# Kernel tuning notes

Hardware: AMD Instinct MI355X
Metric: run time of the kernel (lower is better)

The kernel has to match this reference:

```python
import jax, jax.numpy as jnp
import numpy as np

VOX = 64      # vox_size
KS = 21       # smooth_ks (odd -> 'SAME' == pad ks//2)
SIGMA = 3.0   # smooth_sigma


def smoothing_kernel():
    # normalized 1D gaussian used separably along the 3 voxel axes
    x = jnp.arange(KS, dtype=jnp.float32) - (KS - 1) / 2.0
    g = jnp.exp(-(x * x) / (2.0 * SIGMA * SIGMA))
    return g / g.sum()


def pc_voxels(pc, size):
    """Trilinear scatter of points in [-0.5,0.5]^3 into a [B,size,size,size] grid."""
    B, N, _ = pc.shape
    g = (pc + 0.5) * (size - 1)            # grid coords
    fl = jnp.floor(g)
    idx = fl.astype(jnp.int32)             # [B,N,3] lower corner
    frac = g - fl                          # trilinear fractions
    # 8 corner offsets in {0,1}^3
    offs = jnp.array([[(i >> 2) & 1, (i >> 1) & 1, i & 1] for i in range(8)], dtype=jnp.int32)
    pos = idx[:, :, None, :] + offs[None, None]                       # [B,N,8,3]
    w = jnp.prod(jnp.where(offs[None, None].astype(bool),
                           frac[:, :, None, :], 1.0 - frac[:, :, None, :]), axis=-1)  # [B,N,8]
    inb = jnp.all((pos >= 0) & (pos < size), axis=-1)
    w = jnp.where(inb, w, 0.0)
    posc = jnp.clip(pos, 0, size - 1)
    # voxel layout vox[b, z, y, x]; pc columns are (x, y, z)
    flat = posc[..., 2] * (size * size) + posc[..., 1] * size + posc[..., 0]
    vox = jnp.zeros((B, size * size * size), pc.dtype)
    vox = vox.at[jnp.arange(B)[:, None, None], flat].add(w)
    return jnp.clip(vox.reshape(B, size, size, size), 0.0, 1.0)


def voxels_smooth(v, g1d, scale):
    """Separable 3D Gaussian smoothing + per-batch scale, clamped to [0,1]."""
    x = v[:, None]  # NCDHW, C=1
    ks = g1d.shape[0]
    for kshape in ((1, 1, ks, 1, 1), (1, 1, 1, ks, 1), (1, 1, 1, 1, ks)):
        x = jax.lax.conv_general_dilated(
            x, g1d.reshape(kshape), (1, 1, 1), 'SAME',
            dimension_numbers=('NCDHW', 'OIDHW', 'NCDHW'))
    x = x[:, 0] * scale[:, None, None, None]
    return jnp.clip(x, 0.0, 1.0)


def drc_prob(v):
    """DRC ray-termination probabilities along depth (axis 1)."""
    trans = jnp.cumprod(1.0 - v, axis=1)                                   # [B,D,H,W]
    tshift = jnp.concatenate([jnp.ones_like(trans[:, :1]), trans[:, :-1]], axis=1)
    stop = v * tshift                                                      # stop at voxel d
    esc = trans[:, -1:]                                                    # ray escapes
    return jnp.concatenate([stop, esc], axis=1)                            # [B,D+1,H,W]


def reference(pc, rotation, scale):
    pc_t = jnp.einsum('bni,bji->bnj', pc, rotation)   # camera transform: pc @ R^T
    vox = pc_voxels(pc_t, VOX)
    sm = voxels_smooth(vox, smoothing_kernel(), scale)
    prob = drc_prob(sm)
    proj = prob[:, :-1].sum(1)[:, ::-1, :]            # sum over depth, flip rows
    return proj


def setup_inputs() -> dict:
    key = jax.random.key(0)
    k1, k2, k3 = jax.random.split(key, 3)
    B, N = 32, 65536
    pc = jax.random.uniform(k1, (B, N, 3), jnp.float32) - 0.5   # points in [-0.5, 0.5]
    q, _ = jnp.linalg.qr(jax.random.normal(k2, (B, 3, 3), jnp.float32))  # random rotations
    scale = 0.5 + jax.random.uniform(k3, (B,), jnp.float32)
    return {"pc": pc, "rotation": q, "scale": scale}
```

## Files before the change

kernel.cpp:

```cpp
#include <hip/hip_runtime.h>

#define NB    32
#define NP    65536
#define SZ    64
#define SZ3   (SZ * SZ * SZ)
#define KS    21
#define HALF  10
#define NBIN2 130
#define CAP2  1280
#define FXS   960.0f

typedef _Float16 half8_t __attribute__((ext_vector_type(8)));
typedef _Float16 half4_t __attribute__((ext_vector_type(4)));
typedef float    f32x4_t __attribute__((ext_vector_type(4)));

__device__ __forceinline__ int swz(int row, int col) {
    return (row << 6) + ((((col >> 3) ^ (row & 7))) << 3) + (col & 7);
}

__device__ __forceinline__ void weights_reg(float* w) {
    float sum = 0.0f;
#pragma unroll
    for (int k = 0; k < KS; ++k) {
        float d = (float)k - (float)HALF;
        w[k] = expf(-d * d / 18.0f);
        sum += w[k];
    }
#pragma unroll
    for (int k = 0; k < KS; ++k) w[k] /= sum;
}

__device__ __forceinline__ void fma4(float4& a, float t, const float4& v) {
    a.x = fmaf(t, v.x, a.x); a.y = fmaf(t, v.y, a.y);
    a.z = fmaf(t, v.z, a.z); a.w = fmaf(t, v.w, a.w);
}

__device__ __forceinline__ unsigned pack_fx(float g) {
    float c = fminf(fmaxf(g, -2.0f), 65.0f);
    return (unsigned)__float2uint_rn((c + 2.0f) * FXS);
}

__global__ void fill_kernel(const float* __restrict__ pc,
                            const float* __restrict__ rot,
                            int* __restrict__ cur,
                            uint2* __restrict__ binned,
                            _Float16* __restrict__ Gg) {
    __shared__ int h[4][NBIN2];
    __shared__ int woff[4][NBIN2];
    __shared__ int lbase[NBIN2];
    int base = blockIdx.x * 1024;
    int b = base >> 16;
    int wv = threadIdx.x >> 6;
    for (int i = threadIdx.x; i < 4 * NBIN2; i += 256) h[i / NBIN2][i % NBIN2] = 0;
    __syncthreads();
    const float* R = rot + b * 9;
    const float4* p4 = (const float4*)(pc + (size_t)base * 3);
    float4 f0 = p4[threadIdx.x * 3 + 0];
    float4 f1 = p4[threadIdx.x * 3 + 1];
    float4 f2 = p4[threadIdx.x * 3 + 2];
    float px[4] = {f0.x, f0.w, f1.z, f2.y};
    float py[4] = {f0.y, f1.x, f1.w, f2.z};
    float pz[4] = {f0.z, f1.y, f2.x, f2.w};
    uint2 pk[4];
    int bin0[4], bin1[4], lp0[4], lp1[4];
#pragma unroll
    for (int j = 0; j < 4; ++j) {
        float g0 = (R[0] * px[j] + R[1] * py[j] + R[2] * pz[j] + 0.5f) * 63.0f;
        float g1 = (R[3] * px[j] + R[4] * py[j] + R[5] * pz[j] + 0.5f) * 63.0f;
        float g2 = (R[6] * px[j] + R[7] * py[j] + R[8] * pz[j] + 0.5f) * 63.0f;
        int i2 = (int)floorf(g2);
        int i1 = (int)floorf(g1);
        bool zv = (i2 >= -1 && i2 <= 63);
        int h0 = ((unsigned)i1       < 64u) ? (i1 >> 5)       : -1;
        int h1 = ((unsigned)(i1 + 1) < 64u) ? ((i1 + 1) >> 5) : -1;
        if (h1 == h0) h1 = -1;
        bin0[j] = (zv && h0 >= 0) ? ((i2 + 1) * 2 + h0) : -1;
        bin1[j] = (zv && h1 >= 0) ? ((i2 + 1) * 2 + h1) : -1;
        pk[j] = make_uint2(pack_fx(g0) | (pack_fx(g1) << 16), pack_fx(g2));
        if (bin0[j] >= 0) lp0[j] = atomicAdd(&h[wv][bin0[j]], 1);
        if (bin1[j] >= 0) lp1[j] = atomicAdd(&h[wv][bin1[j]], 1);
    }
    __syncthreads();
    if (threadIdx.x < NBIN2) {
        int t = threadIdx.x;
        int s0 = h[0][t], s1 = h[1][t], s2 = h[2][t], s3 = h[3][t];
        int tot = s0 + s1 + s2 + s3;
        lbase[t] = tot ? atomicAdd(&cur[b * NBIN2 + t], tot) : 0;
        woff[0][t] = 0; woff[1][t] = s0; woff[2][t] = s0 + s1; woff[3][t] = s0 + s1 + s2;
    }
    __syncthreads();
#pragma unroll
    for (int j = 0; j < 4; ++j) {
        if (bin0[j] >= 0) {
            int pos = lbase[bin0[j]] + woff[wv][bin0[j]] + lp0[j];
            if (pos < CAP2)
                binned[(size_t)(b * NBIN2 + bin0[j]) * CAP2 + pos] = pk[j];
        }
        if (bin1[j] >= 0) {
            int pos = lbase[bin1[j]] + woff[wv][bin1[j]] + lp1[j];
            if (pos < CAP2)
                binned[(size_t)(b * NBIN2 + bin1[j]) * CAP2 + pos] = pk[j];
        }
    }
    if (blockIdx.x == 0) {
        float w[KS];
        weights_reg(w);
        for (int i = threadIdx.x; i < 4096; i += 256) {
            int d = (i >> 6) - (i & 63) + HALF;
            Gg[i] = ((unsigned)d < (unsigned)KS) ? (_Float16)w[d] : (_Float16)0.0f;
        }
    }
}

__global__ void __launch_bounds__(128) splat_blur(const uint2* __restrict__ binned,
                                                  const int* __restrict__ cur,
                                                  const _Float16* __restrict__ Gg,
                                                  _Float16* __restrict__ vox) {
    __shared__ __align__(16) char smem[25088];
    int tid = threadIdx.x;
    int w = tid >> 6, lane = tid & 63;
    int idx = blockIdx.x;
    int b = idx >> 6;
    int k = (idx + (b << 3)) & 63;
    int z = (k & 1) ? (31 - (k >> 1)) : (32 + (k >> 1));
    int q = lane >> 4, c = lane & 15;

    _Float16* Ay = (_Float16*)(smem + w * 4224);
    _Float16* Bx = (_Float16*)(smem + 8448 + w * 8320);
    _Float16* P  = (_Float16*)smem;
    _Float16* T  = (_Float16*)(smem + 8448);

    {
        int4 z4 = {0, 0, 0, 0};
        int4* a4 = (int4*)Ay;
        for (int i = lane; i < 4224 / 16; i += 64) a4[i] = z4;
        int4* b4 = (int4*)Bx;
        for (int i = lane; i < 8320 / 16; i += 64) b4[i] = z4;
    }

    half8_t gf[4][2];
#pragma unroll
    for (int ni = 0; ni < 4; ++ni)
#pragma unroll
        for (int hh = 0; hh < 2; ++hh)
            gf[ni][hh] = *(const half8_t*)&Gg[(ni * 16 + c) * 64 + hh * 32 + q * 8];

    int c0 = min(cur[b * NBIN2 + 2 * z + w],       CAP2);
    int c1 = min(cur[b * NBIN2 + 2 * (z + 1) + w], CAP2);
    const uint2* s0 = binned + (size_t)(b * NBIN2 + 2 * z + w) * CAP2;
    const uint2* s1 = binned + (size_t)(b * NBIN2 + 2 * (z + 1) + w) * CAP2;
    int n = c0 + c1;

    f32x4_t acc[2][4];
#pragma unroll
    for (int ml = 0; ml < 2; ++ml)
#pragma unroll
        for (int ni = 0; ni < 4; ++ni) acc[ml][ni] = (f32x4_t){0.f, 0.f, 0.f, 0.f};

    int iters = (n + 63) >> 6;
    uint2 nxtA = make_uint2(0u, 0u), nxtB = make_uint2(0u, 0u);
    {
        int i0g = lane;
        if (i0g < n) nxtA = (i0g < c0) ? s0[i0g] : s1[i0g - c0];
        int i1g = 64 + lane;
        if (i1g < n) nxtB = (i1g < c0) ? s0[i1g] : s1[i1g - c0];
    }
    for (int it = 0; it < iters; ++it) {
        uint2 pk = nxtA;
        nxtA = nxtB;
        nxtB = make_uint2(0u, 0u);
        int ni2 = (it + 2) * 64 + lane;
        if (ni2 < n) nxtB = (ni2 < c0) ? s0[ni2] : s1[ni2 - c0];

        float gx = (float)(pk.x & 0xffffu) * (1.0f / FXS) - 2.0f;
        float gy = (float)(pk.x >> 16)     * (1.0f / FXS) - 2.0f;
        float gz = (float)(pk.y & 0xffffu) * (1.0f / FXS) - 2.0f;
        float f0 = floorf(gx), f1 = floorf(gy);
        int   i0 = (int)f0,    i1 = (int)f1;
        float r0 = gx - f0,    r1f = gy - f1;
        float az = fmaxf(0.0f, 1.0f - fabsf(gz - (float)z));
        int rlo = i1 - (w << 5), rhi = i1 + 1 - (w << 5);
        int alo = ((unsigned)rlo < 32u) ? rlo : 32;
        int ahi = ((unsigned)rhi < 32u) ? rhi : 32;
        int xlo = ((unsigned)i0       < 64u) ? i0       : 64;
        int xhi = ((unsigned)(i0 + 1) < 64u) ? (i0 + 1) : 64;
        Ay[swz(alo, lane)] = (_Float16)(az * (1.0f - r1f));
        Ay[swz(ahi, lane)] = (_Float16)(az * r1f);
        Bx[swz(xlo, lane)] = (_Float16)(1.0f - r0);
        Bx[swz(xhi, lane)] = (_Float16)r0;
#pragma unroll
        for (int hh = 0; hh < 2; ++hh) {
            half8_t af[2], bf[4];
#pragma unroll
            for (int ml = 0; ml < 2; ++ml)
                af[ml] = *(const half8_t*)&Ay[swz(ml * 16 + c, hh * 32 + q * 8)];
#pragma unroll
            for (int ni = 0; ni < 4; ++ni)
                bf[ni] = *(const half8_t*)&Bx[swz(ni * 16 + c, hh * 32 + q * 8)];
#pragma unroll
            for (int ml = 0; ml < 2; ++ml)
#pragma unroll
                for (int ni = 0; ni < 4; ++ni)
                    acc[ml][ni] = __builtin_amdgcn_mfma_f32_16x16x32_f16(
                        af[ml], bf[ni], acc[ml][ni], 0, 0, 0);
        }
        Ay[swz(alo, lane)] = (_Float16)0.0f;
        Ay[swz(ahi, lane)] = (_Float16)0.0f;
        Bx[swz(xlo, lane)] = (_Float16)0.0f;
        Bx[swz(xhi, lane)] = (_Float16)0.0f;
    }

    __syncthreads();

#pragma unroll
    for (int ml = 0; ml < 2; ++ml)
#pragma unroll
        for (int ni = 0; ni < 4; ++ni)
#pragma unroll
            for (int r = 0; r < 4; ++r)
                P[swz((w << 5) + ml * 16 + q * 4 + r, ni * 16 + c)] =
                    (_Float16)fminf(fmaxf(acc[ml][ni][r], 0.0f), 1.0f);
    __syncthreads();

    f32x4_t a2[2][4];
#pragma unroll
    for (int ml = 0; ml < 2; ++ml)
#pragma unroll
        for (int ni = 0; ni < 4; ++ni) a2[ml][ni] = (f32x4_t){0.f, 0.f, 0.f, 0.f};
#pragma unroll
    for (int hh = 0; hh < 2; ++hh) {
        half8_t af[2];
#pragma unroll
        for (int ml = 0; ml < 2; ++ml)
            af[ml] = *(const half8_t*)&P[swz(((w << 1) + ml) * 16 + c, hh * 32 + q * 8)];
#pragma unroll
        for (int ml = 0; ml < 2; ++ml)
#pragma unroll
            for (int ni = 0; ni < 4; ++ni)
                a2[ml][ni] = __builtin_amdgcn_mfma_f32_16x16x32_f16(
                    af[ml], gf[ni][hh], a2[ml][ni], 0, 0, 0);
    }
#pragma unroll
    for (int ml = 0; ml < 2; ++ml)
#pragma unroll
        for (int ni = 0; ni < 4; ++ni) {
            half4_t pkd;
#pragma unroll
            for (int r = 0; r < 4; ++r) pkd[r] = (_Float16)a2[ml][ni][r];
            *(half4_t*)&T[swz(ni * 16 + c, ((w << 1) + ml) * 16 + q * 4)] = pkd;
        }
    __syncthreads();

    f32x4_t a3[2][4];
#pragma unroll
    for (int ml = 0; ml < 2; ++ml)
#pragma unroll
        for (int ni = 0; ni < 4; ++ni) a3[ml][ni] = (f32x4_t){0.f, 0.f, 0.f, 0.f};
#pragma unroll
    for (int hh = 0; hh < 2; ++hh) {
        half8_t bf[4];
#pragma unroll
        for (int ni = 0; ni < 4; ++ni)
            bf[ni] = *(const half8_t*)&T[swz(ni * 16 + c, hh * 32 + q * 8)];
#pragma unroll
        for (int ml = 0; ml < 2; ++ml)
#pragma unroll
            for (int ni = 0; ni < 4; ++ni)
                a3[ml][ni] = __builtin_amdgcn_mfma_f32_16x16x32_f16(
                    gf[(w << 1) + ml][hh], bf[ni], a3[ml][ni], 0, 0, 0);
    }

    _Float16* dst = vox + ((size_t)b << 18) + ((size_t)z << 12);
#pragma unroll
    for (int ml = 0; ml < 2; ++ml)
#pragma unroll
        for (int ni = 0; ni < 4; ++ni)
#pragma unroll
            for (int r = 0; r < 4; ++r)
                dst[(((w << 5) + ml * 16 + q * 4 + r) << 6) + ni * 16 + c] =
                    (_Float16)a3[ml][ni][r];
}

__global__ void convz_drc_kernel(const _Float16* __restrict__ in,
                                 const float* __restrict__ scale,
                                 float* __restrict__ out) {
    __shared__ float sraw[640 + SZ * SZ + 640];
    __shared__ float c[SZ * SZ];
    __shared__ float segS[4][64], segT[4][64];
    float* s = sraw + 640;
    int b = blockIdx.x >> 6, y = blockIdx.x & 63;

    for (int i = threadIdx.x; i < 640; i += 256) {
        sraw[i] = 0.0f;
        sraw[640 + SZ * SZ + i] = 0.0f;
    }
    const _Float16* base = in + ((size_t)b << 18) + (y << 6);
#pragma unroll
    for (int g = 0; g < 4; ++g) {
        int cell = g * 256 + threadIdx.x;
        int z = cell >> 4, xc = (cell & 15) << 2;
        half4_t v = *(const half4_t*)&base[((size_t)z << 12) + xc];
        float4 f = make_float4((float)v[0], (float)v[1], (float)v[2], (float)v[3]);
        *(float4*)&s[(z << 6) + xc] = f;
    }
    __syncthreads();

    float w[KS];
    weights_reg(w);

    {
        int z0 = (threadIdx.x >> 4) << 2;
        int xc = (threadIdx.x & 15) << 2;
        float4 a0 = {0,0,0,0}, a1 = {0,0,0,0}, a2 = {0,0,0,0}, a3 = {0,0,0,0};
#pragma unroll
        for (int d = 0; d < 24; ++d) {
            int zz = z0 - HALF + d;
            float4 v = *(const float4*)&s[(zz << 6) + xc];
            if (d <= 20)           fma4(a0, w[d],     v);
            if (d >= 1 && d <= 21) fma4(a1, w[d - 1], v);
            if (d >= 2 && d <= 22) fma4(a2, w[d - 2], v);
            if (d >= 3)            fma4(a3, w[d - 3], v);
        }
        *(float4*)&c[((z0 + 0) << 6) + xc] = a0;
        *(float4*)&c[((z0 + 1) << 6) + xc] = a1;
        *(float4*)&c[((z0 + 2) << 6) + xc] = a2;
        *(float4*)&c[((z0 + 3) << 6) + xc] = a3;
    }
    __syncthreads();

    {
        int x = threadIdx.x & 63, seg = threadIdx.x >> 6;
        float sc = scale[b];
        float trans = 1.0f, sum = 0.0f;
#pragma unroll
        for (int zz = 0; zz < 16; ++zz) {
            int z = seg * 16 + zz;
            float v = fminf(fmaxf(c[(z << 6) + x] * sc, 0.0f), 1.0f);
            sum += v * trans;
            trans *= 1.0f - v;
        }
        segS[seg][x] = sum;
        segT[seg][x] = trans;
    }
    __syncthreads();
    if (threadIdx.x < 64) {
        int x = threadIdx.x;
        float t = 1.0f, S = 0.0f;
#pragma unroll
        for (int sgi = 0; sgi < 4; ++sgi) { S += segS[sgi][x] * t; t *= segT[sgi][x]; }
        out[(b << 12) + ((63 - y) << 6) + x] = S;
    }
}

extern "C" void kernel_launch(void* const* d_in, const int* in_sizes, int n_in,
                              void* d_out, int out_size, void* d_ws, size_t ws_size,
                              hipStream_t stream) {
    const float* pc    = (const float*)d_in[0];
    const float* rot   = (const float*)d_in[1];
    const float* scale = (const float*)d_in[2];
    float* out = (float*)d_out;

    _Float16* vox    = (_Float16*)d_ws;
    uint2*    binned = (uint2*)((char*)d_ws + (size_t)NB * SZ3 * sizeof(_Float16));
    _Float16* Gg     = (_Float16*)((char*)binned + (size_t)NB * NBIN2 * CAP2 * sizeof(uint2));
    int*      cur    = (int*)((char*)Gg + 64 * 64 * sizeof(_Float16));

    hipMemsetAsync(cur, 0, NB * NBIN2 * sizeof(int), stream);

    fill_kernel     <<<NB * NP / 1024, 256, 0, stream>>>(pc, rot, cur, binned, Gg);
    splat_blur      <<<NB * SZ, 128, 0, stream>>>(binned, cur, Gg, vox);
    convz_drc_kernel<<<NB * SZ, 256, 0, stream>>>(vox, scale, out);
}
```

Before: 121.7 us.

## Bin points into y/x quadrants and use four waves per slice in splat_blur

```diff
diff --git a/kernel.cpp b/kernel.cpp
--- a/kernel.cpp
+++ b/kernel.cpp
@@ -6,8 +6,8 @@
 #define SZ3   (SZ * SZ * SZ)
 #define KS    21
 #define HALF  10
-#define NBIN2 130
-#define CAP2  1280
+#define NBIN4 260
+#define CAP4  1024
 #define FXS   960.0f
 
 typedef _Float16 half8_t __attribute__((ext_vector_type(8)));
@@ -45,13 +45,13 @@
                             int* __restrict__ cur,
                             uint2* __restrict__ binned,
                             _Float16* __restrict__ Gg) {
-    __shared__ int h[4][NBIN2];
-    __shared__ int woff[4][NBIN2];
-    __shared__ int lbase[NBIN2];
+    __shared__ int h[4][NBIN4];
+    __shared__ int woff[4][NBIN4];
+    __shared__ int lbase[NBIN4];
     int base = blockIdx.x * 1024;
     int b = base >> 16;
     int wv = threadIdx.x >> 6;
-    for (int i = threadIdx.x; i < 4 * NBIN2; i += 256) h[i / NBIN2][i % NBIN2] = 0;
+    for (int i = threadIdx.x; i < 4 * NBIN4; i += 256) h[i / NBIN4][i % NBIN4] = 0;
     __syncthreads();
     const float* R = rot + b * 9;
     const float4* p4 = (const float4*)(pc + (size_t)base * 3);
@@ -62,7 +62,7 @@
     float py[4] = {f0.y, f1.x, f1.w, f2.z};
     float pz[4] = {f0.z, f1.y, f2.x, f2.w};
     uint2 pk[4];
-    int bin0[4], bin1[4], lp0[4], lp1[4];
+    int bn[4][4], lp[4][4];
 #pragma unroll
     for (int j = 0; j < 4; ++j) {
         float g0 = (R[0] * px[j] + R[1] * py[j] + R[2] * pz[j] + 0.5f) * 63.0f;
@@ -70,36 +70,41 @@
         float g2 = (R[6] * px[j] + R[7] * py[j] + R[8] * pz[j] + 0.5f) * 63.0f;
         int i2 = (int)floorf(g2);
         int i1 = (int)floorf(g1);
+        int i0 = (int)floorf(g0);
         bool zv = (i2 >= -1 && i2 <= 63);
         int h0 = ((unsigned)i1       < 64u) ? (i1 >> 5)       : -1;
         int h1 = ((unsigned)(i1 + 1) < 64u) ? ((i1 + 1) >> 5) : -1;
         if (h1 == h0) h1 = -1;
-        bin0[j] = (zv && h0 >= 0) ? ((i2 + 1) * 2 + h0) : -1;
-        bin1[j] = (zv && h1 >= 0) ? ((i2 + 1) * 2 + h1) : -1;
+        int v0 = ((unsigned)i0       < 64u) ? (i0 >> 5)       : -1;
+        int v1 = ((unsigned)(i0 + 1) < 64u) ? ((i0 + 1) >> 5) : -1;
+        if (v1 == v0) v1 = -1;
+        int zb = (i2 + 1) * 2;
+        bn[j][0] = (zv && h0 >= 0 && v0 >= 0) ? ((zb + h0) * 2 + v0) : -1;
+        bn[j][1] = (zv && h0 >= 0 && v1 >= 0) ? ((zb + h0) * 2 + v1) : -1;
+        bn[j][2] = (zv && h1 >= 0 && v0 >= 0) ? ((zb + h1) * 2 + v0) : -1;
+        bn[j][3] = (zv && h1 >= 0 && v1 >= 0) ? ((zb + h1) * 2 + v1) : -1;
         pk[j] = make_uint2(pack_fx(g0) | (pack_fx(g1) << 16), pack_fx(g2));
-        if (bin0[j] >= 0) lp0[j] = atomicAdd(&h[wv][bin0[j]], 1);
-        if (bin1[j] >= 0) lp1[j] = atomicAdd(&h[wv][bin1[j]], 1);
-    }
-    __syncthreads();
-    if (threadIdx.x < NBIN2) {
-        int t = threadIdx.x;
+#pragma unroll
+        for (int t = 0; t < 4; ++t)
+            if (bn[j][t] >= 0) lp[j][t] = atomicAdd(&h[wv][bn[j][t]], 1);
+    }
+    __syncthreads();
+    for (int t = threadIdx.x; t < NBIN4; t += 256) {
         int s0 = h[0][t], s1 = h[1][t], s2 = h[2][t], s3 = h[3][t];
         int tot = s0 + s1 + s2 + s3;
-        lbase[t] = tot ? atomicAdd(&cur[b * NBIN2 + t], tot) : 0;
+        lbase[t] = tot ? atomicAdd(&cur[b * NBIN4 + t], tot) : 0;
         woff[0][t] = 0; woff[1][t] = s0; woff[2][t] = s0 + s1; woff[3][t] = s0 + s1 + s2;
     }
     __syncthreads();
 #pragma unroll
     for (int j = 0; j < 4; ++j) {
-        if (bin0[j] >= 0) {
-            int pos = lbase[bin0[j]] + woff[wv][bin0[j]] + lp0[j];
-            if (pos < CAP2)
-                binned[(size_t)(b * NBIN2 + bin0[j]) * CAP2 + pos] = pk[j];
-        }
-        if (bin1[j] >= 0) {
-            int pos = lbase[bin1[j]] + woff[wv][bin1[j]] + lp1[j];
-            if (pos < CAP2)
-                binned[(size_t)(b * NBIN2 + bin1[j]) * CAP2 + pos] = pk[j];
+#pragma unroll
+        for (int t = 0; t < 4; ++t) {
+            if (bn[j][t] >= 0) {
+                int pos = lbase[bn[j][t]] + woff[wv][bn[j][t]] + lp[j][t];
+                if (pos < CAP4)
+                    binned[(size_t)(b * NBIN4 + bn[j][t]) * CAP4 + pos] = pk[j];
+            }
         }
     }
     if (blockIdx.x == 0) {
@@ -112,13 +117,14 @@
     }
 }
 
-__global__ void __launch_bounds__(128) splat_blur(const uint2* __restrict__ binned,
-                                                  const int* __restrict__ cur,
-                                                  const _Float16* __restrict__ Gg,
-                                                  _Float16* __restrict__ vox) {
-    __shared__ __align__(16) char smem[25088];
+__global__ void __launch_bounds__(256, 4) splat_blur(const uint2* __restrict__ binned,
+                                                     const int* __restrict__ cur,
+                                                     const _Float16* __restrict__ Gg,
+                                                     _Float16* __restrict__ vox) {
+    __shared__ __align__(16) char smem[33792];
     int tid = threadIdx.x;
     int w = tid >> 6, lane = tid & 63;
+    int yh = w >> 1, xh = w & 1;
     int idx = blockIdx.x;
     int b = idx >> 6;
     int k = (idx + (b << 3)) & 63;
@@ -126,36 +132,31 @@
     int q = lane >> 4, c = lane & 15;
 
     _Float16* Ay = (_Float16*)(smem + w * 4224);
-    _Float16* Bx = (_Float16*)(smem + 8448 + w * 8320);
+    _Float16* Bx = (_Float16*)(smem + 16896 + w * 4224);
     _Float16* P  = (_Float16*)smem;
-    _Float16* T  = (_Float16*)(smem + 8448);
+    _Float16* T  = (_Float16*)(smem + 16896);
 
     {
         int4 z4 = {0, 0, 0, 0};
         int4* a4 = (int4*)Ay;
         for (int i = lane; i < 4224 / 16; i += 64) a4[i] = z4;
         int4* b4 = (int4*)Bx;
-        for (int i = lane; i < 8320 / 16; i += 64) b4[i] = z4;
-    }
-
-    half8_t gf[4][2];
-#pragma unroll
-    for (int ni = 0; ni < 4; ++ni)
-#pragma unroll
-        for (int hh = 0; hh < 2; ++hh)
-            gf[ni][hh] = *(const half8_t*)&Gg[(ni * 16 + c) * 64 + hh * 32 + q * 8];
-
-    int c0 = min(cur[b * NBIN2 + 2 * z + w],       CAP2);
-    int c1 = min(cur[b * NBIN2 + 2 * (z + 1) + w], CAP2);
-    const uint2* s0 = binned + (size_t)(b * NBIN2 + 2 * z + w) * CAP2;
-    const uint2* s1 = binned + (size_t)(b * NBIN2 + 2 * (z + 1) + w) * CAP2;
+        for (int i = lane; i < 4224 / 16; i += 64) b4[i] = z4;
+    }
+
+    int bin0 = (2 * z + yh) * 2 + xh;
+    int bin1 = (2 * (z + 1) + yh) * 2 + xh;
+    int c0 = min(cur[b * NBIN4 + bin0], CAP4);
+    int c1 = min(cur[b * NBIN4 + bin1], CAP4);
+    const uint2* s0 = binned + (size_t)(b * NBIN4 + bin0) * CAP4;
+    const uint2* s1 = binned + (size_t)(b * NBIN4 + bin1) * CAP4;
     int n = c0 + c1;
 
-    f32x4_t acc[2][4];
+    f32x4_t acc[2][2];
 #pragma unroll
     for (int ml = 0; ml < 2; ++ml)
 #pragma unroll
-        for (int ni = 0; ni < 4; ++ni) acc[ml][ni] = (f32x4_t){0.f, 0.f, 0.f, 0.f};
+        for (int ni = 0; ni < 2; ++ni) acc[ml][ni] = (f32x4_t){0.f, 0.f, 0.f, 0.f};
 
     int iters = (n + 63) >> 6;
     uint2 nxtA = make_uint2(0u, 0u), nxtB = make_uint2(0u, 0u);
@@ -179,28 +180,29 @@
         int   i0 = (int)f0,    i1 = (int)f1;
         float r0 = gx - f0,    r1f = gy - f1;
         float az = fmaxf(0.0f, 1.0f - fabsf(gz - (float)z));
-        int rlo = i1 - (w << 5), rhi = i1 + 1 - (w << 5);
+        int rlo = i1 - (yh << 5), rhi = rlo + 1;
         int alo = ((unsigned)rlo < 32u) ? rlo : 32;
         int ahi = ((unsigned)rhi < 32u) ? rhi : 32;
-        int xlo = ((unsigned)i0       < 64u) ? i0       : 64;
-        int xhi = ((unsigned)(i0 + 1) < 64u) ? (i0 + 1) : 64;
+        int xg  = i0 - (xh << 5);
+        int xlo = ((unsigned)xg       < 32u) ? xg       : 32;
+        int xhi = ((unsigned)(xg + 1) < 32u) ? (xg + 1) : 32;
         Ay[swz(alo, lane)] = (_Float16)(az * (1.0f - r1f));
         Ay[swz(ahi, lane)] = (_Float16)(az * r1f);
         Bx[swz(xlo, lane)] = (_Float16)(1.0f - r0);
         Bx[swz(xhi, lane)] = (_Float16)r0;
 #pragma unroll
         for (int hh = 0; hh < 2; ++hh) {
-            half8_t af[2], bf[4];
+            half8_t af[2], bf[2];
 #pragma unroll
             for (int ml = 0; ml < 2; ++ml)
                 af[ml] = *(const half8_t*)&Ay[swz(ml * 16 + c, hh * 32 + q * 8)];
 #pragma unroll
-            for (int ni = 0; ni < 4; ++ni)
+            for (int ni = 0; ni < 2; ++ni)
                 bf[ni] = *(const half8_t*)&Bx[swz(ni * 16 + c, hh * 32 + q * 8)];
 #pragma unroll
             for (int ml = 0; ml < 2; ++ml)
 #pragma unroll
-                for (int ni = 0; ni < 4; ++ni)
+                for (int ni = 0; ni < 2; ++ni)
                     acc[ml][ni] = __builtin_amdgcn_mfma_f32_16x16x32_f16(
                         af[ml], bf[ni], acc[ml][ni], 0, 0, 0);
         }
@@ -212,73 +214,64 @@
 
     __syncthreads();
 
+    half8_t gf[4][2];
+#pragma unroll
+    for (int ni = 0; ni < 4; ++ni)
+#pragma unroll
+        for (int hh = 0; hh < 2; ++hh)
+            gf[ni][hh] = *(const half8_t*)&Gg[(ni * 16 + c) * 64 + hh * 32 + q * 8];
+
 #pragma unroll
     for (int ml = 0; ml < 2; ++ml)
 #pragma unroll
+        for (int ni = 0; ni < 2; ++ni)
+#pragma unroll
+            for (int r = 0; r < 4; ++r)
+                P[swz((yh << 5) + ml * 16 + q * 4 + r, (xh << 5) + ni * 16 + c)] =
+                    (_Float16)fminf(fmaxf(acc[ml][ni][r], 0.0f), 1.0f);
+    __syncthreads();
+
+    f32x4_t a2[4];
+#pragma unroll
+    for (int ni = 0; ni < 4; ++ni) a2[ni] = (f32x4_t){0.f, 0.f, 0.f, 0.f};
+#pragma unroll
+    for (int hh = 0; hh < 2; ++hh) {
+        half8_t af1 = *(const half8_t*)&P[swz(w * 16 + c, hh * 32 + q * 8)];
+#pragma unroll
         for (int ni = 0; ni < 4; ++ni)
-#pragma unroll
-            for (int r = 0; r < 4; ++r)
-                P[swz((w << 5) + ml * 16 + q * 4 + r, ni * 16 + c)] =
-                    (_Float16)fminf(fmaxf(acc[ml][ni][r], 0.0f), 1.0f);
-    __syncthreads();
-
-    f32x4_t a2[2][4];
-#pragma unroll
-    for (int ml = 0; ml < 2; ++ml)
-#pragma unroll
-        for (int ni = 0; ni < 4; ++ni) a2[ml][ni] = (f32x4_t){0.f, 0.f, 0.f, 0.f};
+            a2[ni] = __builtin_amdgcn_mfma_f32_16x16x32_f16(
+                af1, gf[ni][hh], a2[ni], 0, 0, 0);
+    }
+#pragma unroll
+    for (int ni = 0; ni < 4; ++ni) {
+        half4_t pkd;
+#pragma unroll
+        for (int r = 0; r < 4; ++r) pkd[r] = (_Float16)a2[ni][r];
+        *(half4_t*)&T[swz(ni * 16 + c, w * 16 + q * 4)] = pkd;
+    }
+    __syncthreads();
+
+    f32x4_t a3[4];
+#pragma unroll
+    for (int ni = 0; ni < 4; ++ni) a3[ni] = (f32x4_t){0.f, 0.f, 0.f, 0.f};
 #pragma unroll
     for (int hh = 0; hh < 2; ++hh) {
-        half8_t af[2];
-#pragma unroll
-        for (int ml = 0; ml < 2; ++ml)
-            af[ml] = *(const half8_t*)&P[swz(((w << 1) + ml) * 16 + c, hh * 32 + q * 8)];
-#pragma unroll
-        for (int ml = 0; ml < 2; ++ml)
-#pragma unroll
-            for (int ni = 0; ni < 4; ++ni)
-                a2[ml][ni] = __builtin_amdgcn_mfma_f32_16x16x32_f16(
-                    af[ml], gf[ni][hh], a2[ml][ni], 0, 0, 0);
-    }
-#pragma unroll
-    for (int ml = 0; ml < 2; ++ml)
-#pragma unroll
-        for (int ni = 0; ni < 4; ++ni) {
-            half4_t pkd;
-#pragma unroll
-            for (int r = 0; r < 4; ++r) pkd[r] = (_Float16)a2[ml][ni][r];
-            *(half4_t*)&T[swz(ni * 16 + c, ((w << 1) + ml) * 16 + q * 4)] = pkd;
-        }
-    __syncthreads();
-
-    f32x4_t a3[2][4];
-#pragma unroll
-    for (int ml = 0; ml < 2; ++ml)
-#pragma unroll
-        for (int ni = 0; ni < 4; ++ni) a3[ml][ni] = (f32x4_t){0.f, 0.f, 0.f, 0.f};
-#pragma unroll
-    for (int hh = 0; hh < 2; ++hh) {
-        half8_t bf[4];
+        half8_t bf1[4];
 #pragma unroll
         for (int ni = 0; ni < 4; ++ni)
-            bf[ni] = *(const half8_t*)&T[swz(ni * 16 + c, hh * 32 + q * 8)];
-#pragma unroll
-        for (int ml = 0; ml < 2; ++ml)
-#pragma unroll
-            for (int ni = 0; ni < 4; ++ni)
-                a3[ml][ni] = __builtin_amdgcn_mfma_f32_16x16x32_f16(
-                    gf[(w << 1) + ml][hh], bf[ni], a3[ml][ni], 0, 0, 0);
+            bf1[ni] = *(const half8_t*)&T[swz(ni * 16 + c, hh * 32 + q * 8)];
+#pragma unroll
+        for (int ni = 0; ni < 4; ++ni)
+            a3[ni] = __builtin_amdgcn_mfma_f32_16x16x32_f16(
+                gf[w][hh], bf1[ni], a3[ni], 0, 0, 0);
     }
 
     _Float16* dst = vox + ((size_t)b << 18) + ((size_t)z << 12);
 #pragma unroll
-    for (int ml = 0; ml < 2; ++ml)
-#pragma unroll
-        for (int ni = 0; ni < 4; ++ni)
-#pragma unroll
-            for (int r = 0; r < 4; ++r)
-                dst[(((w << 5) + ml * 16 + q * 4 + r) << 6) + ni * 16 + c] =
-                    (_Float16)a3[ml][ni][r];
+    for (int ni = 0; ni < 4; ++ni)
+#pragma unroll
+        for (int r = 0; r < 4; ++r)
+            dst[((w * 16 + q * 4 + r) << 6) + ni * 16 + c] = (_Float16)a3[ni][r];
 }
 
 __global__ void convz_drc_kernel(const _Float16* __restrict__ in,
@@ -362,12 +355,12 @@
 
     _Float16* vox    = (_Float16*)d_ws;
     uint2*    binned = (uint2*)((char*)d_ws + (size_t)NB * SZ3 * sizeof(_Float16));
-    _Float16* Gg     = (_Float16*)((char*)binned + (size_t)NB * NBIN2 * CAP2 * sizeof(uint2));
+    _Float16* Gg     = (_Float16*)((char*)binned + (size_t)NB * NBIN4 * CAP4 * sizeof(uint2));
     int*      cur    = (int*)((char*)Gg + 64 * 64 * sizeof(_Float16));
 
-    hipMemsetAsync(cur, 0, NB * NBIN2 * sizeof(int), stream);
+    hipMemsetAsync(cur, 0, NB * NBIN4 * sizeof(int), stream);
 
     fill_kernel     <<<NB * NP / 1024, 256, 0, stream>>>(pc, rot, cur, binned, Gg);
-    splat_blur      <<<NB * SZ, 128, 0, stream>>>(binned, cur, Gg, vox);
+    splat_blur      <<<NB * SZ, 256, 0, stream>>>(binned, cur, Gg, vox);
     convz_drc_kernel<<<NB * SZ, 256, 0, stream>>>(vox, scale, out);
 }
```

After: 137.0 us. +12.6%, slower.

## Precompute splat indices and fp16 weights in fill kernel, shrinking splat inner loop

Applied to the files above, without the earlier changes.

```diff
diff --git a/kernel.cpp b/kernel.cpp
--- a/kernel.cpp
+++ b/kernel.cpp
@@ -8,14 +8,17 @@
 #define HALF  10
 #define NBIN2 130
 #define CAP2  1280
-#define FXS   960.0f
 
 typedef _Float16 half8_t __attribute__((ext_vector_type(8)));
 typedef _Float16 half4_t __attribute__((ext_vector_type(4)));
+typedef _Float16 half2_t __attribute__((ext_vector_type(2)));
 typedef float    f32x4_t __attribute__((ext_vector_type(4)));
 
 __device__ __forceinline__ int swz(int row, int col) {
     return (row << 6) + ((((col >> 3) ^ (row & 7))) << 3) + (col & 7);
+}
+__device__ __forceinline__ int swzl(int row, int lane) {
+    return (((row << 6) | ((row & 7) << 3)) ^ lane);
 }
 
 __device__ __forceinline__ void weights_reg(float* w) {
@@ -35,15 +38,15 @@
     a.z = fmaf(t, v.z, a.z); a.w = fmaf(t, v.w, a.w);
 }
 
-__device__ __forceinline__ unsigned pack_fx(float g) {
-    float c = fminf(fmaxf(g, -2.0f), 65.0f);
-    return (unsigned)__float2uint_rn((c + 2.0f) * FXS);
+__device__ __forceinline__ unsigned h16(float x) {
+    _Float16 h = (_Float16)x;
+    return (unsigned)__builtin_bit_cast(unsigned short, h);
 }
 
 __global__ void fill_kernel(const float* __restrict__ pc,
                             const float* __restrict__ rot,
                             int* __restrict__ cur,
-                            uint2* __restrict__ binned,
+                            uint4* __restrict__ binned,
                             _Float16* __restrict__ Gg) {
     __shared__ int h[4][NBIN2];
     __shared__ int woff[4][NBIN2];
@@ -61,22 +64,38 @@
     float px[4] = {f0.x, f0.w, f1.z, f2.y};
     float py[4] = {f0.y, f1.x, f1.w, f2.z};
     float pz[4] = {f0.z, f1.y, f2.x, f2.w};
-    uint2 pk[4];
+    uint4 pk[4][2];
     int bin0[4], bin1[4], lp0[4], lp1[4];
 #pragma unroll
     for (int j = 0; j < 4; ++j) {
         float g0 = (R[0] * px[j] + R[1] * py[j] + R[2] * pz[j] + 0.5f) * 63.0f;
         float g1 = (R[3] * px[j] + R[4] * py[j] + R[5] * pz[j] + 0.5f) * 63.0f;
         float g2 = (R[6] * px[j] + R[7] * py[j] + R[8] * pz[j] + 0.5f) * 63.0f;
-        int i2 = (int)floorf(g2);
-        int i1 = (int)floorf(g1);
+        float fl0 = floorf(g0), fl1 = floorf(g1), fl2 = floorf(g2);
+        int i0 = (int)fl0, i1 = (int)fl1, i2 = (int)fl2;
+        float r0 = g0 - fl0, r1 = g1 - fl1, fz = g2 - fl2;
         bool zv = (i2 >= -1 && i2 <= 63);
         int h0 = ((unsigned)i1       < 64u) ? (i1 >> 5)       : -1;
         int h1 = ((unsigned)(i1 + 1) < 64u) ? ((i1 + 1) >> 5) : -1;
         if (h1 == h0) h1 = -1;
         bin0[j] = (zv && h0 >= 0) ? ((i2 + 1) * 2 + h0) : -1;
         bin1[j] = (zv && h1 >= 0) ? ((i2 + 1) * 2 + h1) : -1;
-        pk[j] = make_uint2(pack_fx(g0) | (pack_fx(g1) << 16), pack_fx(g2));
+
+        int xlo = ((unsigned)i0       < 64u) ? i0       : 64;
+        int xhi = ((unsigned)(i0 + 1) < 64u) ? (i0 + 1) : 64;
+        unsigned xw = ((unsigned)xlo << 16) | ((unsigned)xhi << 24);
+        unsigned ey = h16(fz)        | (h16(1.0f - fz) << 16);
+        unsigned ez = h16(1.0f - r1) | (h16(r1)        << 16);
+        unsigned ew = h16(1.0f - r0) | (h16(r0)        << 16);
+#pragma unroll
+        for (int s = 0; s < 2; ++s) {
+            int hh = s ? h1 : h0;
+            int rlo = i1 - ((hh > 0) << 5);
+            int alo = ((unsigned)rlo       < 32u) ? rlo       : 32;
+            int ahi = ((unsigned)(rlo + 1) < 32u) ? (rlo + 1) : 32;
+            pk[j][s].x = (unsigned)alo | ((unsigned)ahi << 8) | xw;
+            pk[j][s].y = ey; pk[j][s].z = ez; pk[j][s].w = ew;
+        }
         if (bin0[j] >= 0) lp0[j] = atomicAdd(&h[wv][bin0[j]], 1);
         if (bin1[j] >= 0) lp1[j] = atomicAdd(&h[wv][bin1[j]], 1);
     }
@@ -94,12 +113,12 @@
         if (bin0[j] >= 0) {
             int pos = lbase[bin0[j]] + woff[wv][bin0[j]] + lp0[j];
             if (pos < CAP2)
-                binned[(size_t)(b * NBIN2 + bin0[j]) * CAP2 + pos] = pk[j];
+                binned[(size_t)(b * NBIN2 + bin0[j]) * CAP2 + pos] = pk[j][0];
         }
         if (bin1[j] >= 0) {
             int pos = lbase[bin1[j]] + woff[wv][bin1[j]] + lp1[j];
             if (pos < CAP2)
-                binned[(size_t)(b * NBIN2 + bin1[j]) * CAP2 + pos] = pk[j];
+                binned[(size_t)(b * NBIN2 + bin1[j]) * CAP2 + pos] = pk[j][1];
         }
     }
     if (blockIdx.x == 0) {
@@ -112,7 +131,7 @@
     }
 }
 
-__global__ void __launch_bounds__(128) splat_blur(const uint2* __restrict__ binned,
+__global__ void __launch_bounds__(128) splat_blur(const uint4* __restrict__ binned,
                                                   const int* __restrict__ cur,
                                                   const _Float16* __restrict__ Gg,
                                                   _Float16* __restrict__ vox) {
@@ -138,17 +157,9 @@
         for (int i = lane; i < 8320 / 16; i += 64) b4[i] = z4;
     }
 
-    half8_t gf[4][2];
-#pragma unroll
-    for (int ni = 0; ni < 4; ++ni)
-#pragma unroll
-        for (int hh = 0; hh < 2; ++hh)
-            gf[ni][hh] = *(const half8_t*)&Gg[(ni * 16 + c) * 64 + hh * 32 + q * 8];
-
     int c0 = min(cur[b * NBIN2 + 2 * z + w],       CAP2);
     int c1 = min(cur[b * NBIN2 + 2 * (z + 1) + w], CAP2);
-    const uint2* s0 = binned + (size_t)(b * NBIN2 + 2 * z + w) * CAP2;
-    const uint2* s1 = binned + (size_t)(b * NBIN2 + 2 * (z + 1) + w) * CAP2;
+    const uint4* s0 = binned + (size_t)(b * NBIN2 + 2 * z + w) * CAP2;
     int n = c0 + c1;
 
     f32x4_t acc[2][4];
@@ -157,37 +168,35 @@
 #pragma unroll
         for (int ni = 0; ni < 4; ++ni) acc[ml][ni] = (f32x4_t){0.f, 0.f, 0.f, 0.f};
 
+    const uint4 pkz = make_uint4(0x40402020u, 0u, 0u, 0u);
     int iters = (n + 63) >> 6;
-    uint2 nxtA = make_uint2(0u, 0u), nxtB = make_uint2(0u, 0u);
+    uint4 nxtA = pkz, nxtB = pkz;
+    int fA = 0, fB = 0;
     {
         int i0g = lane;
-        if (i0g < n) nxtA = (i0g < c0) ? s0[i0g] : s1[i0g - c0];
+        if (i0g < n) { fA = i0g >= c0; nxtA = s0[i0g + (fA ? 2 * CAP2 - c0 : 0)]; }
         int i1g = 64 + lane;
-        if (i1g < n) nxtB = (i1g < c0) ? s0[i1g] : s1[i1g - c0];
+        if (i1g < n) { fB = i1g >= c0; nxtB = s0[i1g + (fB ? 2 * CAP2 - c0 : 0)]; }
     }
     for (int it = 0; it < iters; ++it) {
-        uint2 pk = nxtA;
-        nxtA = nxtB;
-        nxtB = make_uint2(0u, 0u);
+        uint4 pk = nxtA; int fk = fA;
+        nxtA = nxtB; fA = fB;
+        nxtB = pkz; fB = 0;
         int ni2 = (it + 2) * 64 + lane;
-        if (ni2 < n) nxtB = (ni2 < c0) ? s0[ni2] : s1[ni2 - c0];
-
-        float gx = (float)(pk.x & 0xffffu) * (1.0f / FXS) - 2.0f;
-        float gy = (float)(pk.x >> 16)     * (1.0f / FXS) - 2.0f;
-        float gz = (float)(pk.y & 0xffffu) * (1.0f / FXS) - 2.0f;
-        float f0 = floorf(gx), f1 = floorf(gy);
-        int   i0 = (int)f0,    i1 = (int)f1;
-        float r0 = gx - f0,    r1f = gy - f1;
-        float az = fmaxf(0.0f, 1.0f - fabsf(gz - (float)z));
-        int rlo = i1 - (w << 5), rhi = i1 + 1 - (w << 5);
-        int alo = ((unsigned)rlo < 32u) ? rlo : 32;
-        int ahi = ((unsigned)rhi < 32u) ? rhi : 32;
-        int xlo = ((unsigned)i0       < 64u) ? i0       : 64;
-        int xhi = ((unsigned)(i0 + 1) < 64u) ? (i0 + 1) : 64;
-        Ay[swz(alo, lane)] = (_Float16)(az * (1.0f - r1f));
-        Ay[swz(ahi, lane)] = (_Float16)(az * r1f);
-        Bx[swz(xlo, lane)] = (_Float16)(1.0f - r0);
-        Bx[swz(xhi, lane)] = (_Float16)r0;
+        if (ni2 < n) { fB = ni2 >= c0; nxtB = s0[ni2 + (fB ? 2 * CAP2 - c0 : 0)]; }
+
+        int alo = pk.x & 0xff, ahi = (pk.x >> 8) & 0xff;
+        int xlo = (pk.x >> 16) & 0xff, xhi = pk.x >> 24;
+        unsigned azu = fk ? (pk.y >> 16) : (pk.y & 0xffffu);
+        half2_t az2 = __builtin_bit_cast(half2_t, azu | (azu << 16));
+        half2_t ay2 = az2 * __builtin_bit_cast(half2_t, pk.z);
+        half2_t bx2 = __builtin_bit_cast(half2_t, pk.w);
+        int aAlo = swzl(alo, lane), aAhi = swzl(ahi, lane);
+        int aXlo = swzl(xlo, lane), aXhi = swzl(xhi, lane);
+        Ay[aAlo] = ay2.x;
+        Ay[aAhi] = ay2.y;
+        Bx[aXlo] = bx2.x;
+        Bx[aXhi] = bx2.y;
 #pragma unroll
         for (int hh = 0; hh < 2; ++hh) {
             half8_t af[2], bf[4];
@@ -204,13 +213,20 @@
                     acc[ml][ni] = __builtin_amdgcn_mfma_f32_16x16x32_f16(
                         af[ml], bf[ni], acc[ml][ni], 0, 0, 0);
         }
-        Ay[swz(alo, lane)] = (_Float16)0.0f;
-        Ay[swz(ahi, lane)] = (_Float16)0.0f;
-        Bx[swz(xlo, lane)] = (_Float16)0.0f;
-        Bx[swz(xhi, lane)] = (_Float16)0.0f;
-    }
-
-    __syncthreads();
+        Ay[aAlo] = (_Float16)0.0f;
+        Ay[aAhi] = (_Float16)0.0f;
+        Bx[aXlo] = (_Float16)0.0f;
+        Bx[aXhi] = (_Float16)0.0f;
+    }
+
+    __syncthreads();
+
+    half8_t gf[4][2];
+#pragma unroll
+    for (int ni = 0; ni < 4; ++ni)
+#pragma unroll
+        for (int hh = 0; hh < 2; ++hh)
+            gf[ni][hh] = *(const half8_t*)&Gg[(ni * 16 + c) * 64 + hh * 32 + q * 8];
 
 #pragma unroll
     for (int ml = 0; ml < 2; ++ml)
@@ -361,8 +377,8 @@
     float* out = (float*)d_out;
 
     _Float16* vox    = (_Float16*)d_ws;
-    uint2*    binned = (uint2*)((char*)d_ws + (size_t)NB * SZ3 * sizeof(_Float16));
-    _Float16* Gg     = (_Float16*)((char*)binned + (size_t)NB * NBIN2 * CAP2 * sizeof(uint2));
+    uint4*    binned = (uint4*)((char*)d_ws + (size_t)NB * SZ3 * sizeof(_Float16));
+    _Float16* Gg     = (_Float16*)((char*)binned + (size_t)NB * NBIN2 * CAP2 * sizeof(uint4));
     int*      cur    = (int*)((char*)Gg + 64 * 64 * sizeof(_Float16));
 
     hipMemsetAsync(cur, 0, NB * NBIN2 * sizeof(int), stream);
```

After: 126.5 us. +4.0%, slower.
